# Kernel tuning notes

Measured on AMD Instinct MI355X. Metric: run time of the kernel, lower is better.

The kernel has to match this reference:

```python
import jax, jax.numpy as jnp
import numpy as np

CROP = 224      # args.image_size
RESIZE_MAX = 1024


def setup_inputs() -> dict:
    key = jax.random.key(0)
    k1, k2, k3, k4, k5 = jax.random.split(key, 5)
    x = jax.random.normal(k1, (8, 3, 16, 512, 512), dtype=jnp.float32)
    cam_views = jax.random.randint(k2, (8,), 0, 3)  # Dashboard/Right_side_window/Rear_view
    # learned parameters (float, initialized as in torch randint inits)
    resize = jax.random.randint(k3, (3,), CROP, RESIZE_MAX).astype(jnp.float32)
    y_offset = jax.random.randint(k4, (3,), 0, 32).astype(jnp.float32)
    x_offset = jax.random.randint(k5, (3,), 0, 32).astype(jnp.float32)
    return {"x": x, "cam_views": cam_views, "resize": resize,
            "y_offset": y_offset, "x_offset": x_offset}


def _coords(off, rb, H):
    # Fused resize+crop source coordinates (align_corners=False):
    # dst pixel i of the crop sits at (off + i) in the virtual resized image;
    # its source coord in the original H-sized axis is (dst+0.5)*H/r - 0.5.
    i = jnp.arange(CROP, dtype=jnp.float32)
    src = (off[:, None] + i[None, :] + 0.5) * (H / rb[:, None]) - 0.5  # [B, S]
    src = jnp.maximum(src, 0.0)  # torch clamps negative source index to 0
    i0 = jnp.clip(jnp.floor(src).astype(jnp.int32), 0, H - 1)
    i1 = jnp.minimum(i0 + 1, H - 1)
    w = src - i0.astype(src.dtype)
    return i0, i1, w


def _sample_clip(clip, y0, y1, wy, x0, x1, wx):
    # clip: [C, T, H, W]; bilinear gather of only the crop window's samples
    rows = clip[:, :, y0, :] * (1.0 - wy)[:, None] + clip[:, :, y1, :] * wy[:, None]  # [C,T,S,W]
    return rows[:, :, :, x0] * (1.0 - wx) + rows[:, :, :, x1] * wx  # [C,T,S,S]


def reference(x, cam_views, resize, y_offset, x_offset):
    H = x.shape[3]
    # torch: clamp then .type(int16) (truncation, non-differentiable)
    r = jax.lax.stop_gradient(jnp.floor(jnp.clip(resize, H, RESIZE_MAX)))
    yo = jax.lax.stop_gradient(jnp.floor(jnp.clip(y_offset, 0.0, r - CROP)))
    xo = jax.lax.stop_gradient(jnp.floor(jnp.clip(x_offset, 0.0, r - CROP)))
    rb = r[cam_views]  # per-clip resize  [B]
    y0, y1, wy = _coords(yo[cam_views], rb, H)
    x0, x1, wx = _coords(xo[cam_views], rb, H)
    prompt = jax.vmap(_sample_clip)(x, y0, y1, wy, x0, x1, wx)  # [B,C,T,S,S]
    return prompt
```

## Files before the change

kernel.cpp:

```cpp
#include <hip/hip_runtime.h>


#define CROP   224
#define HSZ    512
#define QPR    56
#define IMGS   (8 * 3 * 16)
#define TOTAL_THREADS (IMGS * CROP * QPR)

__global__ __launch_bounds__(256) void crop_prompter_kernel(
    const float* __restrict__ x,
    const int*   __restrict__ cam_views,
    const float* __restrict__ resize,
    const float* __restrict__ y_off,
    const float* __restrict__ x_off,
    float*       __restrict__ out)
{
    const int tid = blockIdx.x * blockDim.x + threadIdx.x;

    const int q   = tid % QPR;
    const int t1  = tid / QPR;
    const int sy  = t1 % CROP;
    const int img = t1 / CROP;
    const int b   = img / 48;

    const int v = cam_views[b];
    const float r  = floorf(fminf(fmaxf(resize[v], 512.0f), 1024.0f));
    const float yo = floorf(fminf(fmaxf(y_off[v], 0.0f), r - 224.0f));
    const float xo = floorf(fminf(fmaxf(x_off[v], 0.0f), r - 224.0f));
    const float scale = 512.0f / r;

    float srcy = (yo + (float)sy + 0.5f) * scale - 0.5f;
    srcy = fmaxf(srcy, 0.0f);
    int y0 = (int)floorf(srcy);
    y0 = min(max(y0, 0), HSZ - 1);
    const int y1 = min(y0 + 1, HSZ - 1);
    const float wy  = srcy - (float)y0;
    const float wyc = 1.0f - wy;

    const float* __restrict__ row0 = x + ((size_t)img * HSZ + (size_t)y0) * HSZ;
    const float* __restrict__ row1 = x + ((size_t)img * HSZ + (size_t)y1) * HSZ;

    float4 res;
    float* rp = reinterpret_cast<float*>(&res);

#pragma unroll
    for (int j = 0; j < 4; ++j) {
        const int sx = q * 4 + j;
        float srcx = (xo + (float)sx + 0.5f) * scale - 0.5f;
        srcx = fmaxf(srcx, 0.0f);
        int x0 = (int)floorf(srcx);
        x0 = min(max(x0, 0), HSZ - 1);
        const float wx = srcx - (float)x0;

        const int x0c = min(x0, HSZ - 2);
        float2 t2, b2;
        __builtin_memcpy(&t2, row0 + x0c, sizeof(float2));
        __builtin_memcpy(&b2, row1 + x0c, sizeof(float2));

        const bool edge = (x0 == HSZ - 1);
        const float v00 = edge ? t2.y : t2.x;
        const float v10 = edge ? b2.y : b2.x;
        const float v01 = t2.y;
        const float v11 = b2.y;

        const float left  = v00 * wyc + v10 * wy;
        const float right = v01 * wyc + v11 * wy;
        rp[j] = left * (1.0f - wx) + right * wx;
    }

    reinterpret_cast<float4*>(out)[tid] = res;
}

extern "C" void kernel_launch(void* const* d_in, const int* in_sizes, int n_in,
                              void* d_out, int out_size, void* d_ws, size_t ws_size,
                              hipStream_t stream) {
    const float* x         = (const float*)d_in[0];
    const int*   cam_views = (const int*)  d_in[1];
    const float* resize    = (const float*)d_in[2];
    const float* y_off     = (const float*)d_in[3];
    const float* x_off     = (const float*)d_in[4];
    float* out = (float*)d_out;

    const int block = 256;
    const int grid  = TOTAL_THREADS / block;

    crop_prompter_kernel<<<grid, block, 0, stream>>>(
        x, cam_views, resize, y_off, x_off, out);
}
```

Baseline: 491.0 us.

## Stage source row spans in LDS per output row with XCD-aware block mapping

Each block now handles one output row. It loads the two needed source-row spans into shared memory with coalesced float4 loads, and each of 224 threads then interpolates one pixel from LDS. Block IDs are remapped so consecutive rows land on the same XCD, which improves L2 reuse of adjacent source rows. The cost is a syncthreads per block, idle threads (only 224 of 256 active, fewer for loads), and scalar instead of vectorized output stores.

```diff
diff --git a/kernel.cpp b/kernel.cpp
--- a/kernel.cpp
+++ b/kernel.cpp
@@ -3,9 +3,12 @@
 
 #define CROP   224
 #define HSZ    512
-#define QPR    56
-#define IMGS   (8 * 3 * 16)
-#define TOTAL_THREADS (IMGS * CROP * QPR)
+#define NIMG   (8 * 3 * 16)
+#define NROWS  (NIMG * CROP)
+#define NXCD   8
+#define CHUNK  (NROWS / NXCD)
+#define MAXQ   58
+#define MAXSPAN (MAXQ * 4)
 
 __global__ __launch_bounds__(256) void crop_prompter_kernel(
     const float* __restrict__ x,
@@ -15,60 +18,64 @@
     const float* __restrict__ x_off,
     float*       __restrict__ out)
 {
-    const int tid = blockIdx.x * blockDim.x + threadIdx.x;
+    __shared__ float lds[2][MAXSPAN];
 
-    const int q   = tid % QPR;
-    const int t1  = tid / QPR;
-    const int sy  = t1 % CROP;
-    const int img = t1 / CROP;
+    const int bid = (int)blockIdx.x;
+    const int s   = (bid & (NXCD - 1)) * CHUNK + (bid >> 3);
+
+    const int sy  = s % CROP;
+    const int img = s / CROP;
     const int b   = img / 48;
 
     const int v = cam_views[b];
     const float r  = floorf(fminf(fmaxf(resize[v], 512.0f), 1024.0f));
-    const float yo = floorf(fminf(fmaxf(y_off[v], 0.0f), r - 224.0f));
-    const float xo = floorf(fminf(fmaxf(x_off[v], 0.0f), r - 224.0f));
+    const float yo = floorf(fminf(fmaxf(y_off[v],  0.0f), r - 224.0f));
+    const float xo = floorf(fminf(fmaxf(x_off[v],  0.0f), r - 224.0f));
     const float scale = 512.0f / r;
 
-    float srcy = (yo + (float)sy + 0.5f) * scale - 0.5f;
-    srcy = fmaxf(srcy, 0.0f);
-    int y0 = (int)floorf(srcy);
-    y0 = min(max(y0, 0), HSZ - 1);
-    const int y1 = min(y0 + 1, HSZ - 1);
+    float srcy = fmaxf((yo + (float)sy + 0.5f) * scale - 0.5f, 0.0f);
+    const int   y0  = min((int)srcy, HSZ - 1);
+    const int   y1  = min(y0 + 1, HSZ - 1);
     const float wy  = srcy - (float)y0;
     const float wyc = 1.0f - wy;
 
-    const float* __restrict__ row0 = x + ((size_t)img * HSZ + (size_t)y0) * HSZ;
-    const float* __restrict__ row1 = x + ((size_t)img * HSZ + (size_t)y1) * HSZ;
+    const float srcx0 = fmaxf((xo +   0.5f) * scale - 0.5f, 0.0f);
+    const float srcxL = fmaxf((xo + 223.5f) * scale - 0.5f, 0.0f);
+    const int xf   = min((int)srcx0, HSZ - 2) & ~3;
+    const int end4 = (min((int)srcxL, HSZ - 2) + 2 + 3) & ~3;
+    const int n4   = (end4 - xf) >> 2;
 
-    float4 res;
-    float* rp = reinterpret_cast<float*>(&res);
+    const float* __restrict__ base = x + (size_t)img * (HSZ * HSZ);
 
-#pragma unroll
-    for (int j = 0; j < 4; ++j) {
-        const int sx = q * 4 + j;
-        float srcx = (xo + (float)sx + 0.5f) * scale - 0.5f;
-        srcx = fmaxf(srcx, 0.0f);
-        int x0 = (int)floorf(srcx);
-        x0 = min(max(x0, 0), HSZ - 1);
+    const int t = (int)threadIdx.x;
+    if (t < 2 * n4) {
+        const int rowsel = (t >= n4) ? 1 : 0;
+        const int qi     = t - (rowsel ? n4 : 0);
+        const int yr     = rowsel ? y1 : y0;
+        float4 q;
+        __builtin_memcpy(&q, base + (size_t)yr * HSZ + xf + 4 * qi, sizeof(float4));
+        *reinterpret_cast<float4*>(&lds[rowsel][4 * qi]) = q;
+    }
+    __syncthreads();
+
+    if (t < CROP) {
+        float srcx = fmaxf((xo + (float)t + 0.5f) * scale - 0.5f, 0.0f);
+        const int   x0 = min((int)srcx, HSZ - 1);
         const float wx = srcx - (float)x0;
+        const int   x0c = min(x0, HSZ - 2);
+        const int   li  = x0c - xf;
 
-        const int x0c = min(x0, HSZ - 2);
-        float2 t2, b2;
-        __builtin_memcpy(&t2, row0 + x0c, sizeof(float2));
-        __builtin_memcpy(&b2, row1 + x0c, sizeof(float2));
+        const float t0 = lds[0][li], t1 = lds[0][li + 1];
+        const float b0 = lds[1][li], b1 = lds[1][li + 1];
 
-        const bool edge = (x0 == HSZ - 1);
-        const float v00 = edge ? t2.y : t2.x;
-        const float v10 = edge ? b2.y : b2.x;
-        const float v01 = t2.y;
-        const float v11 = b2.y;
+        const bool  edge = (x0 == HSZ - 1);
+        const float v00  = edge ? t1 : t0;
+        const float v10  = edge ? b1 : b0;
 
         const float left  = v00 * wyc + v10 * wy;
-        const float right = v01 * wyc + v11 * wy;
-        rp[j] = left * (1.0f - wx) + right * wx;
+        const float right = t1  * wyc + b1  * wy;
+        out[((size_t)img * CROP + sy) * CROP + t] = left * (1.0f - wx) + right * wx;
     }
-
-    reinterpret_cast<float4*>(out)[tid] = res;
 }
 
 extern "C" void kernel_launch(void* const* d_in, const int* in_sizes, int n_in,
@@ -81,9 +88,6 @@
     const float* x_off     = (const float*)d_in[4];
     float* out = (float*)d_out;
 
-    const int block = 256;
-    const int grid  = TOTAL_THREADS / block;
-
-    crop_prompter_kernel<<<grid, block, 0, stream>>>(
+    crop_prompter_kernel<<<NROWS, 256, 0, stream>>>(
         x, cam_views, resize, y_off, x_off, out);
 }
```

After: 511.8 us. +4.2%, slower.
